# Performance work log

Hardware: AMD Instinct MI355X
Metric: run time of the kernel (lower is better)

The kernel has to match this reference:

```python
import jax, jax.numpy as jnp
import numpy as np

N_NODE = 40000
EMB = 100
LAYERS = 2
B = 512
L = 50
N = 50
E = 800000


def _l2norm(x, axis=-1, eps=1e-12):
    n = jnp.sqrt(jnp.sum(x * x, axis=axis, keepdims=True))
    return x / jnp.maximum(n, eps)


def _item_conv(rows, cols, vals, emb, b):
    # sparse A @ X repeated LAYERS times, stack, l2-normalize rows, weighted sum
    finals = [emb]
    x = emb
    for _ in range(LAYERS):
        x = jax.ops.segment_sum(vals[:, None] * x[cols], rows, num_segments=emb.shape[0])
        finals.append(x)
    f = _l2norm(jnp.stack(finals, 0))                      # [LAYERS+1, n, d]
    return jnp.sum(b[:, None, None] * f, axis=0)


def _session_conv(adj_dense, emb, a):
    finals = [emb]
    x = emb
    for _ in range(LAYERS):
        x = adj_dense @ x
        finals.append(x)
    f = _l2norm(jnp.stack(finals, 0))
    return jnp.sum(a[:, None, None] * f, axis=0)


def _gat(h, adj, a0, a1, a2, a3):
    # e_k[b,i,j] = leakyrelu(sum_d h[b,i,d]*h[b,j,d]*a_k[d]); never materialize [B,N,N,D]
    def score(a):
        return jax.nn.leaky_relu(jnp.einsum('bid,bjd->bij', h * a[:, 0], h), 0.2)
    e0, e1, e2, e3 = score(a0), score(a1), score(a2), score(a3)
    neg = jnp.float32(-9e15)
    alpha = jnp.where(adj == 1, e0, neg)
    alpha = jnp.where(adj == 2, e1, alpha)
    alpha = jnp.where(adj == 3, e2, alpha)
    alpha = jnp.where(adj == 4, e3, alpha)
    alpha = jax.nn.softmax(alpha, axis=-1)
    return jnp.einsum('bij,bjd->bid', alpha, h)


def _get_seq(emb_table, rev, h, alias, mix=0.8):
    seq_h = emb_table[rev]                                  # [B,L,D]
    bidx = jnp.arange(rev.shape[0])[:, None]
    seq_h_ = h[bidx, alias]                                 # [B,L,D]
    return (1.0 - mix) * seq_h + mix * seq_h_               # eval: dropout = identity


def _soft_attention(seq_h, mask_f, session_len, pos_emb, w1_W, w1_b, glu1_W, glu1_b, glu2_W, w2):
    hs = jnp.sum(seq_h, axis=1) / session_len               # [B,D]
    pos = jnp.broadcast_to(pos_emb[:seq_h.shape[1]][None], seq_h.shape)
    nh = jnp.tanh(jnp.concatenate([pos, seq_h], -1) @ w1_W.T + w1_b)
    nh = jax.nn.sigmoid(nh @ glu1_W.T + glu1_b + (hs @ glu2_W.T)[:, None, :])
    beta = (nh @ w2) * mask_f[..., None]                    # [B,L,1]
    return jnp.sum(beta * seq_h, axis=1)                    # [B,D]


def setup_inputs() -> dict:
    key = jax.random.key(0)
    ks = jax.random.split(key, 30)
    stdv = 1.0 / np.sqrt(EMB)
    u = lambda k, s: jax.random.uniform(k, s, jnp.float32, -stdv, stdv)
    return {
        'tar': jax.random.randint(ks[0], (B,), 0, N_NODE),
        'reversed_sess_item': jax.random.randint(ks[1], (B, L), 0, N_NODE + 1),
        'mask': jnp.ones((B, L), jnp.int32),
        'session_len': jnp.ones((B, 1), jnp.float32),
        'session_adj': jax.random.uniform(ks[2], (B, B), jnp.float32),
        'is_train': 0,
        'items': jax.random.randint(ks[3], (B, N), 0, N_NODE + 1),
        'adj': jax.random.randint(ks[4], (B, N, N), 0, 5),
        'alias_session': jax.random.randint(ks[5], (B, L), 0, N),
        'gnn_rows': jax.random.randint(ks[6], (E,), 0, N_NODE),
        'gnn_cols': jax.random.randint(ks[7], (E,), 0, N_NODE),
        'gnn_vals': jax.random.uniform(ks[8], (E,), jnp.float32),
        'nodes_emb': u(ks[9], (N_NODE, EMB)),
        'b_item': jnp.ones((LAYERS + 1,), jnp.float32),
        'a_sess': jnp.ones((LAYERS + 1,), jnp.float32),
        'a0': u(ks[10], (EMB, 1)), 'a1': u(ks[11], (EMB, 1)),
        'a2': u(ks[12], (EMB, 1)), 'a3': u(ks[13], (EMB, 1)),
        'w1_W': u(ks[14], (EMB, 2 * EMB)), 'w1_b': u(ks[15], (EMB,)),
        'w2': u(ks[16], (EMB, 1)),
        'glu1_W': u(ks[17], (EMB, EMB)), 'glu1_b': u(ks[18], (EMB,)),
        'glu2_W': u(ks[19], (EMB, EMB)),
        'pos_emb': u(ks[20], (150, EMB)),
    }


def reference(tar, reversed_sess_item, mask, session_len, session_adj, is_train,
              items, adj, alias_session, gnn_rows, gnn_cols, gnn_vals,
              nodes_emb, b_item, a_sess, a0, a1, a2, a3,
              w1_W, w1_b, w2, glu1_W, glu1_b, glu2_W, pos_emb):
    mask_f = mask.astype(jnp.float32)
    zeros = jnp.zeros((1, EMB), jnp.float32)
    emb_gnn = _item_conv(gnn_rows, gnn_cols, gnn_vals, nodes_emb, b_item)
    # eval mode: both dropouts are identity
    e1t = jnp.concatenate([zeros, emb_gnn], 0)
    e2t = jnp.concatenate([zeros, emb_gnn], 0)
    embeddings = e1t + e2t

    h1 = _gat(e1t[items], adj, a0, a1, a2, a3)
    h1 = _get_seq(e1t, reversed_sess_item, h1, alias_session, 0.8)
    h2 = _gat(e2t[items], adj, a0, a1, a2, a3)
    h2 = _get_seq(e2t, reversed_sess_item, h2, alias_session, 0.8)

    sel1 = _soft_attention(h1, mask_f, session_len, pos_emb, w1_W, w1_b, glu1_W, glu1_b, glu2_W, w2)
    sel1 = _session_conv(session_adj, sel1, a_sess)
    sel2 = _soft_attention(h2, mask_f, session_len, pos_emb, w1_W, w1_b, glu1_W, glu1_b, glu2_W, w2)
    sel2 = _session_conv(session_adj, sel2, a_sess)

    con_loss = jnp.float32(0.0)  # is_train == 0 (inference path)

    seq_h = sel1 + sel2
    scores = seq_h @ embeddings[1:].T                       # [B, N_NODE]
    logp = jax.nn.log_softmax(scores + 1e-8, axis=-1)
    loss = -jnp.mean(logp[jnp.arange(scores.shape[0]), tar])
    return (con_loss, loss, scores)
```

## Files before the change

### kernel.cpp

```cpp
#include <hip/hip_runtime.h>
#include <hip/hip_bf16.h>
#include <math.h>

#define N_NODE 40000
#define EMB 100
#define BB 512
#define LL 50
#define NI 50
#define EDG 800000
#define SCAN_BLOCKS 157

typedef short s16x8 __attribute__((ext_vector_type(8)));
typedef float f32x4 __attribute__((ext_vector_type(4)));

__global__ void khist(const int* __restrict__ rows, int* __restrict__ counts) {
  int e = blockIdx.x * 256 + threadIdx.x;
  atomicAdd(&counts[rows[e]], 1);
}

__global__ __launch_bounds__(256) void kscan1(const int* __restrict__ counts,
                                              int* __restrict__ scanout,
                                              int* __restrict__ blocksums, int n) {
  __shared__ int wsum[4];
  int tid = threadIdx.x;
  int i = blockIdx.x * 256 + tid;
  int v = (i < n) ? counts[i] : 0;
  int x = v;
  #pragma unroll
  for (int off = 1; off < 64; off <<= 1) {
    int t = __shfl_up(x, off, 64);
    if ((tid & 63) >= off) x += t;
  }
  int w = tid >> 6, lane = tid & 63;
  if (lane == 63) wsum[w] = x;
  __syncthreads();
  int woff = 0;
  #pragma unroll
  for (int k = 0; k < 4; ++k) woff += (k < w) ? wsum[k] : 0;
  int incl = x + woff;
  if (i < n) scanout[i] = incl - v;
  if (tid == 255) blocksums[blockIdx.x] = incl;
}

__global__ __launch_bounds__(256) void kscan2(int* __restrict__ blocksums, int nb) {
  __shared__ int wsum[4];
  int tid = threadIdx.x;
  int v = (tid < nb) ? blocksums[tid] : 0;
  int x = v;
  #pragma unroll
  for (int off = 1; off < 64; off <<= 1) {
    int t = __shfl_up(x, off, 64);
    if ((tid & 63) >= off) x += t;
  }
  int w = tid >> 6, lane = tid & 63;
  if (lane == 63) wsum[w] = x;
  __syncthreads();
  int woff = 0;
  #pragma unroll
  for (int k = 0; k < 4; ++k) woff += (k < w) ? wsum[k] : 0;
  if (tid < nb) blocksums[tid] = x + woff - v;
}

__global__ __launch_bounds__(256) void kscan3(const int* __restrict__ scanout,
                                              const int* __restrict__ blocksums,
                                              int* __restrict__ starts,
                                              int* __restrict__ cursor, int n) {
  int i = blockIdx.x * 256 + threadIdx.x;
  if (i < n) {
    int s = scanout[i] + blocksums[blockIdx.x];
    starts[i] = s;
    cursor[i] = s;
  }
}

__global__ void kfill(const int* __restrict__ rows, const int* __restrict__ cols,
                      const float* __restrict__ vals, int* __restrict__ cursor,
                      int* __restrict__ colS, float* __restrict__ valS) {
  int e = blockIdx.x * 256 + threadIdx.x;
  int r = rows[e];
  int p = atomicAdd(&cursor[r], 1);
  colS[p] = cols[e];
  valS[p] = vals[e];
}

__global__ __launch_bounds__(256) void kspmm(const int* __restrict__ starts,
                                             const int* __restrict__ counts,
                                             const int* __restrict__ colS,
                                             const float* __restrict__ valS,
                                             const float* __restrict__ x,
                                             float* __restrict__ out) {
  int row = blockIdx.x * 4 + (threadIdx.x >> 6);
  int lane = threadIdx.x & 63;
  int s = starts[row], cnt = counts[row];
  bool act = lane < 50;
  int d2 = (act ? lane : 49) * 2;
  float ax = 0.f, ay = 0.f;
  for (int base = 0; base < cnt; base += 64) {
    int nb = cnt - base; if (nb > 64) nb = 64;
    int cl = 0; float vl = 0.f;
    if (lane < nb) {
      cl = colS[s + base + lane];
      vl = valS[s + base + lane];
    }
    int t = 0;
    for (; t + 4 <= nb; t += 4) {
      int c0 = __shfl(cl, t),     c1 = __shfl(cl, t + 1);
      int c2 = __shfl(cl, t + 2), c3 = __shfl(cl, t + 3);
      float v0 = __shfl(vl, t),     v1 = __shfl(vl, t + 1);
      float v2 = __shfl(vl, t + 2), v3 = __shfl(vl, t + 3);
      float2 g0 = *(const float2*)(x + (size_t)c0 * EMB + d2);
      float2 g1 = *(const float2*)(x + (size_t)c1 * EMB + d2);
      float2 g2 = *(const float2*)(x + (size_t)c2 * EMB + d2);
      float2 g3 = *(const float2*)(x + (size_t)c3 * EMB + d2);
      ax += v0 * g0.x; ay += v0 * g0.y;
      ax += v1 * g1.x; ay += v1 * g1.y;
      ax += v2 * g2.x; ay += v2 * g2.y;
      ax += v3 * g3.x; ay += v3 * g3.y;
    }
    for (; t < nb; ++t) {
      int c = __shfl(cl, t);
      float v = __shfl(vl, t);
      float2 g = *(const float2*)(x + (size_t)c * EMB + d2);
      ax += v * g.x; ay += v * g.y;
    }
  }
  if (act) {
    float2 o; o.x = ax; o.y = ay;
    *(float2*)(out + (size_t)row * EMB + d2) = o;
  }
}

__global__ void kcomb(const float* __restrict__ x0, const float* __restrict__ x1,
                      const float* __restrict__ x2, const float* __restrict__ bI,
                      float* __restrict__ emb) {
  int n = blockIdx.x * 4 + (threadIdx.x >> 6);
  int lane = threadIdx.x & 63;
  int d0 = lane, d1 = lane + 64;
  bool h1 = d1 < EMB;
  size_t base = (size_t)n * EMB;
  float v00 = x0[base + d0], v01 = h1 ? x0[base + d1] : 0.f;
  float v10 = x1[base + d0], v11 = h1 ? x1[base + d1] : 0.f;
  float v20 = x2[base + d0], v21 = h1 ? x2[base + d1] : 0.f;
  float q0 = v00 * v00 + v01 * v01;
  float q1 = v10 * v10 + v11 * v11;
  float q2 = v20 * v20 + v21 * v21;
  #pragma unroll
  for (int off = 32; off; off >>= 1) {
    q0 += __shfl_xor(q0, off);
    q1 += __shfl_xor(q1, off);
    q2 += __shfl_xor(q2, off);
  }
  float r0 = 1.f / fmaxf(sqrtf(q0), 1e-12f);
  float r1 = 1.f / fmaxf(sqrtf(q1), 1e-12f);
  float r2 = 1.f / fmaxf(sqrtf(q2), 1e-12f);
  float b0 = bI[0], b1 = bI[1], b2 = bI[2];
  emb[base + d0] = b0 * v00 * r0 + b1 * v10 * r1 + b2 * v20 * r2;
  if (h1) emb[base + d1] = b0 * v01 * r0 + b1 * v11 * r1 + b2 * v21 * r2;
}

__global__ __launch_bounds__(256) void kgat(
    const float* __restrict__ emb, const int* __restrict__ items,
    const int* __restrict__ adj,
    const float* __restrict__ a0p, const float* __restrict__ a1p,
    const float* __restrict__ a2p, const float* __restrict__ a3p,
    float* __restrict__ hgat) {
  __shared__ __align__(16) float hl[64 * 108];
  __shared__ __align__(16) float as[4 * 100];
  __shared__ float al[4][4][64];
  int b = blockIdx.x;
  int tid = threadIdx.x;
  for (int idx = tid; idx < 400; idx += 256) {
    int k = idx / 100, d = idx % 100;
    const float* ap = (k == 0) ? a0p : (k == 1) ? a1p : (k == 2) ? a2p : a3p;
    as[idx] = ap[d];
  }
  for (int idx = tid; idx < 64 * 100; idx += 256) {
    int i = idx / 100, d = idx % 100;
    float v = 0.f;
    if (i < NI) {
      int node = items[b * NI + i];
      v = (node == 0) ? 0.f : emb[(size_t)(node - 1) * EMB + d];
    }
    hl[i * 108 + d] = v;
  }
  __syncthreads();
  int w = tid >> 6, lane = tid & 63;
  int i0 = w * 13;
  int nIw = 50 - i0; if (nIw > 13) nIw = 13;
  const float* hjrow = &hl[lane * 108];
  int u2 = lane >> 5, dq = lane & 31;
  int dqc = (dq < 25) ? dq : 24;
  for (int g = 0; g < nIw; g += 4) {
    int ib = i0 + g;
    int rem = nIw - g;
    int ir[4];
    #pragma unroll
    for (int u = 0; u < 4; ++u) { int i = ib + u; ir[u] = (i < NI) ? i : NI - 1; }
    float acck[4][4];
    #pragma unroll
    for (int u = 0; u < 4; ++u)
      #pragma unroll
      for (int k = 0; k < 4; ++k) acck[u][k] = 0.f;
    for (int d0 = 0; d0 < 100; d0 += 4) {
      float4 hj = *(const float4*)(hjrow + d0);
      float4 av0 = *(const float4*)&as[d0];
      float4 av1 = *(const float4*)&as[100 + d0];
      float4 av2 = *(const float4*)&as[200 + d0];
      float4 av3 = *(const float4*)&as[300 + d0];
      #pragma unroll
      for (int u = 0; u < 4; ++u) {
        float4 hi = *(const float4*)&hl[ir[u] * 108 + d0];
        float p0 = hi.x * hj.x, p1 = hi.y * hj.y;
        float p2 = hi.z * hj.z, p3 = hi.w * hj.w;
        acck[u][0] += p0 * av0.x + p1 * av0.y + p2 * av0.z + p3 * av0.w;
        acck[u][1] += p0 * av1.x + p1 * av1.y + p2 * av1.z + p3 * av1.w;
        acck[u][2] += p0 * av2.x + p1 * av2.y + p2 * av2.z + p3 * av2.w;
        acck[u][3] += p0 * av3.x + p1 * av3.y + p2 * av3.z + p3 * av3.w;
      }
    }
    #pragma unroll
    for (int u = 0; u < 4; ++u) {
      int i = ib + u;
      bool rowok = (u < rem);
      int av = 0;
      if (rowok && lane < NI) av = adj[(size_t)b * (NI * NI) + i * NI + lane];
      float sv = (av == 1) ? acck[u][0] : (av == 2) ? acck[u][1]
               : (av == 3) ? acck[u][2] : acck[u][3];
      sv = (sv >= 0.f) ? sv : 0.2f * sv;
      float e = (av == 0) ? -9e15f : sv;
      if (lane >= NI) e = -INFINITY;
      float m = e;
      #pragma unroll
      for (int off = 32; off; off >>= 1) m = fmaxf(m, __shfl_xor(m, off));
      float p = expf(e - m);
      float s = p;
      #pragma unroll
      for (int off = 32; off; off >>= 1) s += __shfl_xor(s, off);
      al[w][u][lane] = p / s;
    }
    #pragma unroll
    for (int pass = 0; pass < 2; ++pass) {
      int u = pass * 2 + u2;
      int i = ib + u;
      const float* alr = al[w][u];
      float ox = 0.f, oy = 0.f, oz = 0.f, ow = 0.f;
      for (int j = 0; j < NI; ++j) {
        float a = alr[j];
        float4 hv = *(const float4*)&hl[j * 108 + dqc * 4];
        ox += a * hv.x; oy += a * hv.y; oz += a * hv.z; ow += a * hv.w;
      }
      if (dq < 25 && u < rem) {
        float4 o4; o4.x = ox; o4.y = oy; o4.z = oz; o4.w = ow;
        *(float4*)&hgat[((size_t)b * NI + i) * EMB + dq * 4] = o4;
      }
    }
  }
}

__global__ void kseq(const float* __restrict__ emb, const int* __restrict__ rev,
                     const int* __restrict__ alias, const float* __restrict__ hgat,
                     float* __restrict__ hseq) {
  int idx = blockIdx.x * 256 + threadIdx.x;
  int b = idx / 5000, r = idx % 5000, l = r / 100, d = r % 100;
  int node = rev[b * LL + l];
  float sh = (node == 0) ? 0.f : emb[(size_t)(node - 1) * EMB + d];
  int a = alias[b * LL + l];
  float shh = hgat[((size_t)b * NI + a) * EMB + d];
  hseq[idx] = 0.2f * sh + 0.8f * shh;
}

__global__ void kprep_t(const float* __restrict__ w1W, const float* __restrict__ g1W,
                        const float* __restrict__ g2W, float* __restrict__ w1t2,
                        float* __restrict__ g1t, float* __restrict__ g2t) {
  int idx = blockIdx.x * 256 + threadIdx.x;
  if (idx >= 10000) return;
  int c = idx / 100, o = idx % 100;
  w1t2[c * 100 + o] = w1W[o * 200 + 100 + c];
  g1t[c * 100 + o] = g1W[o * 100 + c];
  g2t[c * 100 + o] = g2W[o * 100 + c];
}

__global__ void kprep_pos(const float* __restrict__ posE, const float* __restrict__ w1W,
                          const float* __restrict__ w1b, float* __restrict__ posW) {
  int idx = blockIdx.x * 256 + threadIdx.x;
  if (idx >= 5000) return;
  int l = idx / 100, o = idx % 100;
  float acc = w1b[o];
  for (int c = 0; c < 100; ++c) acc += posE[l * 100 + c] * w1W[o * 200 + c];
  posW[idx] = acc;
}

__global__ __launch_bounds__(256) void ksoft(
    const float* __restrict__ hseqG, const float* __restrict__ slenp,
    const int* __restrict__ maskp,
    const float* __restrict__ posW, const float* __restrict__ w1t2,
    const float* __restrict__ glu1t, const float* __restrict__ glu1b,
    const float* __restrict__ glu2t, const float* __restrict__ w2,
    float* __restrict__ sel) {
  __shared__ float hq[LL * 101];
  __shared__ float nh[LL * 100];
  __shared__ float red[25 * 52];
  __shared__ float hs_s[100];
  __shared__ float g_s[100];
  __shared__ float beta_s[LL];
  int b = blockIdx.x, tid = threadIdx.x;
  for (int idx = tid; idx < LL * 100; idx += 256) {
    int l = idx / 100, d = idx % 100;
    hq[l * 101 + d] = hseqG[((size_t)b * LL + l) * 100 + d];
  }
  __syncthreads();
  if (tid < 100) {
    float s = 0.f;
    for (int l = 0; l < LL; ++l) s += hq[l * 101 + tid];
    hs_s[tid] = s / slenp[b];
  }
  __syncthreads();
  if (tid < 100) {
    float acc = 0.f;
    for (int c = 0; c < 100; ++c) acc += hs_s[c] * glu2t[c * 100 + tid];
    g_s[tid] = acc;
  }
  int lg = tid / 25, og = tid % 25;
  if (tid < 250) {
    float acc[5][4];
    #pragma unroll
    for (int j = 0; j < 5; ++j) {
      float4 p = *(const float4*)&posW[(lg * 5 + j) * 100 + og * 4];
      acc[j][0] = p.x; acc[j][1] = p.y; acc[j][2] = p.z; acc[j][3] = p.w;
    }
    for (int c = 0; c < 100; ++c) {
      float4 wv = *(const float4*)&w1t2[c * 100 + og * 4];
      float hv[5];
      #pragma unroll
      for (int j = 0; j < 5; ++j) hv[j] = hq[(lg * 5 + j) * 101 + c];
      #pragma unroll
      for (int j = 0; j < 5; ++j) {
        acc[j][0] += hv[j] * wv.x;
        acc[j][1] += hv[j] * wv.y;
        acc[j][2] += hv[j] * wv.z;
        acc[j][3] += hv[j] * wv.w;
      }
    }
    #pragma unroll
    for (int j = 0; j < 5; ++j) {
      float4 t;
      t.x = tanhf(acc[j][0]); t.y = tanhf(acc[j][1]);
      t.z = tanhf(acc[j][2]); t.w = tanhf(acc[j][3]);
      *(float4*)&nh[(lg * 5 + j) * 100 + og * 4] = t;
    }
  }
  __syncthreads();
  if (tid < 250) {
    float4 gb = *(const float4*)&glu1b[og * 4];
    float4 gg = *(const float4*)&g_s[og * 4];
    float base0 = gg.x + gb.x, base1 = gg.y + gb.y, base2 = gg.z + gb.z, base3 = gg.w + gb.w;
    float acc[5][4];
    #pragma unroll
    for (int j = 0; j < 5; ++j) {
      acc[j][0] = base0; acc[j][1] = base1; acc[j][2] = base2; acc[j][3] = base3;
    }
    for (int c = 0; c < 100; ++c) {
      float4 wv = *(const float4*)&glu1t[c * 100 + og * 4];
      float hv[5];
      #pragma unroll
      for (int j = 0; j < 5; ++j) hv[j] = nh[(lg * 5 + j) * 100 + c];
      #pragma unroll
      for (int j = 0; j < 5; ++j) {
        acc[j][0] += hv[j] * wv.x;
        acc[j][1] += hv[j] * wv.y;
        acc[j][2] += hv[j] * wv.z;
        acc[j][3] += hv[j] * wv.w;
      }
    }
    float4 w2v = *(const float4*)&w2[og * 4];
    #pragma unroll
    for (int j = 0; j < 5; ++j) {
      float s0 = w2v.x / (1.f + expf(-acc[j][0]));
      float s1 = w2v.y / (1.f + expf(-acc[j][1]));
      float s2 = w2v.z / (1.f + expf(-acc[j][2]));
      float s3 = w2v.w / (1.f + expf(-acc[j][3]));
      red[og * 52 + lg * 5 + j] = (s0 + s1) + (s2 + s3);
    }
  }
  __syncthreads();
  if (tid < LL) {
    float s = 0.f;
    for (int og2 = 0; og2 < 25; ++og2) s += red[og2 * 52 + tid];
    beta_s[tid] = s * (float)maskp[b * LL + tid];
  }
  __syncthreads();
  if (tid < 100) {
    float acc = 0.f;
    for (int l = 0; l < LL; ++l) acc += beta_s[l] * hq[l * 101 + tid];
    sel[(size_t)b * 100 + tid] = acc;
  }
}

__global__ void ksess(const float* __restrict__ adjS, const float* __restrict__ x,
                      float* __restrict__ out) {
  int b = blockIdx.x, d = threadIdx.x;
  if (d >= 100) return;
  const float* ar = adjS + (size_t)b * BB;
  float a0 = 0.f, a1 = 0.f, a2 = 0.f, a3 = 0.f;
  for (int j = 0; j < BB; j += 4) {
    a0 += ar[j]     * x[(j)     * 100 + d];
    a1 += ar[j + 1] * x[(j + 1) * 100 + d];
    a2 += ar[j + 2] * x[(j + 2) * 100 + d];
    a3 += ar[j + 3] * x[(j + 3) * 100 + d];
  }
  out[(size_t)b * 100 + d] = (a0 + a1) + (a2 + a3);
}

__global__ void ksesscomb(const float* __restrict__ x0, const float* __restrict__ x1,
                          const float* __restrict__ x2, const float* __restrict__ aS,
                          float* __restrict__ out) {
  int b = blockIdx.x * 4 + (threadIdx.x >> 6);
  int lane = threadIdx.x & 63;
  int d0 = lane, d1 = lane + 64;
  bool h1 = d1 < EMB;
  size_t base = (size_t)b * EMB;
  float v00 = x0[base + d0], v01 = h1 ? x0[base + d1] : 0.f;
  float v10 = x1[base + d0], v11 = h1 ? x1[base + d1] : 0.f;
  float v20 = x2[base + d0], v21 = h1 ? x2[base + d1] : 0.f;
  float q0 = v00 * v00 + v01 * v01;
  float q1 = v10 * v10 + v11 * v11;
  float q2 = v20 * v20 + v21 * v21;
  #pragma unroll
  for (int off = 32; off; off >>= 1) {
    q0 += __shfl_xor(q0, off);
    q1 += __shfl_xor(q1, off);
    q2 += __shfl_xor(q2, off);
  }
  float r0 = 1.f / fmaxf(sqrtf(q0), 1e-12f);
  float r1 = 1.f / fmaxf(sqrtf(q1), 1e-12f);
  float r2 = 1.f / fmaxf(sqrtf(q2), 1e-12f);
  float b0 = aS[0], b1 = aS[1], b2 = aS[2];
  out[base + d0] = 2.f * (b0 * v00 * r0 + b1 * v10 * r1 + b2 * v20 * r2);
  if (h1) out[base + d1] = 2.f * (b0 * v01 * r0 + b1 * v11 * r1 + b2 * v21 * r2);
}

__global__ void kprepB(const float* __restrict__ emb, unsigned short* __restrict__ bHi,
                       unsigned short* __restrict__ bLo) {
  int idx = blockIdx.x * 256 + threadIdx.x;
  int n = idx >> 7, k = idx & 127;
  float v = (k < EMB) ? 2.f * emb[(size_t)n * EMB + k] : 0.f;
  __hip_bfloat16 h = __float2bfloat16(v);
  float rem = v - __bfloat162float(h);
  __hip_bfloat16 l = __float2bfloat16(rem);
  bHi[idx] = *reinterpret_cast<unsigned short*>(&h);
  bLo[idx] = *reinterpret_cast<unsigned short*>(&l);
}

__global__ void kprepA(const float* __restrict__ seqh, unsigned short* __restrict__ aHi,
                       unsigned short* __restrict__ aLo) {
  int idx = blockIdx.x * 256 + threadIdx.x;
  int n = idx >> 7, k = idx & 127;
  float v = (k < EMB) ? seqh[(size_t)n * EMB + k] : 0.f;
  __hip_bfloat16 h = __float2bfloat16(v);
  float rem = v - __bfloat162float(h);
  __hip_bfloat16 l = __float2bfloat16(rem);
  aHi[idx] = *reinterpret_cast<unsigned short*>(&h);
  aLo[idx] = *reinterpret_cast<unsigned short*>(&l);
}

__global__ __launch_bounds__(256) void kscoresM(
    const unsigned short* __restrict__ aHi, const unsigned short* __restrict__ aLo,
    const unsigned short* __restrict__ bHi, const unsigned short* __restrict__ bLo,
    float* __restrict__ outS) {
  __shared__ __align__(16) unsigned short Bh[64 * 136];
  __shared__ __align__(16) unsigned short Bl[64 * 136];
  int tid = threadIdx.x;
  int n0 = blockIdx.x * 64, b0 = blockIdx.y * 64;
  int w = tid >> 6, lane = tid & 63;
  int ln = lane & 15, quad = lane >> 4;

  const unsigned short* aRowH = aHi + (size_t)(b0 + w * 16 + ln) * 128 + quad * 8;
  const unsigned short* aRowL = aLo + (size_t)(b0 + w * 16 + ln) * 128 + quad * 8;
  s16x8 ah[4], al[4];
  #pragma unroll
  for (int s = 0; s < 4; ++s) {
    ah[s] = *(const s16x8*)(aRowH + s * 32);
    al[s] = *(const s16x8*)(aRowL + s * 32);
  }

  #pragma unroll
  for (int it = 0; it < 4; ++it) {
    int seg = tid + it * 256;
    int r = seg >> 4, q = seg & 15;
    *(s16x8*)&Bh[r * 136 + q * 8] = *(const s16x8*)&bHi[(size_t)(n0 + r) * 128 + q * 8];
    *(s16x8*)&Bl[r * 136 + q * 8] = *(const s16x8*)&bLo[(size_t)(n0 + r) * 128 + q * 8];
  }
  __syncthreads();

  f32x4 acc[4];
  #pragma unroll
  for (int t = 0; t < 4; ++t) acc[t] = (f32x4){0.f, 0.f, 0.f, 0.f};

  #pragma unroll
  for (int s = 0; s < 4; ++s) {
    #pragma unroll
    for (int t = 0; t < 4; ++t) {
      s16x8 bh = *(const s16x8*)&Bh[(t * 16 + ln) * 136 + s * 32 + quad * 8];
      s16x8 bl = *(const s16x8*)&Bl[(t * 16 + ln) * 136 + s * 32 + quad * 8];
      acc[t] = __builtin_amdgcn_mfma_f32_16x16x32_bf16(ah[s], bh, acc[t], 0, 0, 0);
      acc[t] = __builtin_amdgcn_mfma_f32_16x16x32_bf16(al[s], bh, acc[t], 0, 0, 0);
      acc[t] = __builtin_amdgcn_mfma_f32_16x16x32_bf16(ah[s], bl, acc[t], 0, 0, 0);
    }
  }

  int brow = b0 + w * 16 + quad * 4;
  #pragma unroll
  for (int t = 0; t < 4; ++t) {
    int ncol = n0 + t * 16 + ln;
    #pragma unroll
    for (int r = 0; r < 4; ++r) {
      outS[(size_t)(brow + r) * N_NODE + ncol] = acc[t][r];
    }
  }
}

__global__ __launch_bounds__(256) void klse(const float* __restrict__ outS,
                                            const int* __restrict__ tar,
                                            float* __restrict__ part) {
  __shared__ float ms[256], ss[256];
  int b = blockIdx.x, tid = threadIdx.x;
  const float2* sp = (const float2*)(outS + (size_t)b * N_NODE);
  float m = -INFINITY, s = 0.f;
  for (int i = tid; i < N_NODE / 2; i += 256) {
    float2 v = sp[i];
    float mx = fmaxf(v.x, v.y);
    float add = expf(v.x - mx) + expf(v.y - mx);
    if (mx > m) { s = s * expf(m - mx) + add; m = mx; }
    else s += add * expf(mx - m);
  }
  ms[tid] = m; ss[tid] = s;
  __syncthreads();
  for (int st = 128; st; st >>= 1) {
    if (tid < st) {
      float m2 = ms[tid + st], s2 = ss[tid + st];
      float M = fmaxf(ms[tid], m2);
      ss[tid] = ss[tid] * expf(ms[tid] - M) + s2 * expf(m2 - M);
      ms[tid] = M;
    }
    __syncthreads();
  }
  if (tid == 0) {
    float tsc = outS[(size_t)b * N_NODE + tar[b]];
    part[b] = tsc - (ms[0] + logf(ss[0]));
  }
}

__global__ void kfinal(const float* __restrict__ part, float* __restrict__ out) {
  __shared__ float red[256];
  int tid = threadIdx.x;
  red[tid] = part[tid] + part[tid + 256];
  __syncthreads();
  for (int st = 128; st; st >>= 1) {
    if (tid < st) red[tid] += red[tid + st];
    __syncthreads();
  }
  if (tid == 0) {
    out[0] = 0.f;
    out[1] = -red[0] / (float)BB;
  }
}

extern "C" void kernel_launch(void* const* d_in, const int* in_sizes, int n_in,
                              void* d_out, int out_size, void* d_ws, size_t ws_size,
                              hipStream_t stream) {
  const int* tar    = (const int*)d_in[0];
  const int* rev    = (const int*)d_in[1];
  const int* maskp  = (const int*)d_in[2];
  const float* slen = (const float*)d_in[3];
  const float* sadj = (const float*)d_in[4];
  const int* items  = (const int*)d_in[6];
  const int* adjp   = (const int*)d_in[7];
  const int* alias  = (const int*)d_in[8];
  const int* grows  = (const int*)d_in[9];
  const int* gcols  = (const int*)d_in[10];
  const float* gvals = (const float*)d_in[11];
  const float* nemb = (const float*)d_in[12];
  const float* bI   = (const float*)d_in[13];
  const float* aS   = (const float*)d_in[14];
  const float* a0p  = (const float*)d_in[15];
  const float* a1p  = (const float*)d_in[16];
  const float* a2p  = (const float*)d_in[17];
  const float* a3p  = (const float*)d_in[18];
  const float* w1W  = (const float*)d_in[19];
  const float* w1b  = (const float*)d_in[20];
  const float* w2p  = (const float*)d_in[21];
  const float* g1W  = (const float*)d_in[22];
  const float* g1b  = (const float*)d_in[23];
  const float* g2W  = (const float*)d_in[24];
  const float* posE = (const float*)d_in[25];

  float* W = (float*)d_ws;
  size_t o = 0;
  float* emb_gnn = W + o; o += (size_t)N_NODE * EMB;
  float* x1      = W + o; o += (size_t)N_NODE * EMB;
  float* x2      = W + o; o += (size_t)N_NODE * EMB;
  float* sel     = W + o; o += (size_t)BB * EMB;
  float* y1      = W + o; o += (size_t)BB * EMB;
  float* y2      = W + o; o += (size_t)BB * EMB;
  float* seqh    = W + o; o += (size_t)BB * EMB;
  float* posW    = W + o; o += 5120;
  float* w1t2    = W + o; o += 10000;
  float* glu1t   = W + o; o += 10000;
  float* glu2t   = W + o; o += 10000;
  float* valS    = W + o; o += EDG;
  float* part    = W + o; o += 512;
  int* colS   = (int*)(W + o); o += EDG;
  int* counts = (int*)(W + o); o += N_NODE;
  int* starts = (int*)(W + o); o += N_NODE;
  int* cursor = (int*)(W + o); o += N_NODE;
  int* scantmp = (int*)(W + o); o += N_NODE;
  int* blocksums = (int*)(W + o); o += 256;
  unsigned short* aHi = (unsigned short*)(W + o); o += 32768;
  unsigned short* aLo = (unsigned short*)(W + o); o += 32768;
  float* hgat = x1;
  float* hseq = x2;
  unsigned short* bHi = (unsigned short*)x1;
  unsigned short* bLo = (unsigned short*)x2;

  float* outF = (float*)d_out;
  float* outScores = outF + 2;

  hipMemsetAsync(counts, 0, N_NODE * sizeof(int), stream);
  khist<<<EDG / 256, 256, 0, stream>>>(grows, counts);
  kscan1<<<SCAN_BLOCKS, 256, 0, stream>>>(counts, scantmp, blocksums, N_NODE);
  kscan2<<<1, 256, 0, stream>>>(blocksums, SCAN_BLOCKS);
  kscan3<<<SCAN_BLOCKS, 256, 0, stream>>>(scantmp, blocksums, starts, cursor, N_NODE);
  kfill<<<EDG / 256, 256, 0, stream>>>(grows, gcols, gvals, cursor, colS, valS);
  kspmm<<<N_NODE / 4, 256, 0, stream>>>(starts, counts, colS, valS, nemb, x1);
  kspmm<<<N_NODE / 4, 256, 0, stream>>>(starts, counts, colS, valS, x1, x2);
  kcomb<<<N_NODE / 4, 256, 0, stream>>>(nemb, x1, x2, bI, emb_gnn);
  kgat<<<BB, 256, 0, stream>>>(emb_gnn, items, adjp, a0p, a1p, a2p, a3p, hgat);
  kseq<<<(BB * LL * EMB) / 256, 256, 0, stream>>>(emb_gnn, rev, alias, hgat, hseq);
  kprep_t<<<40, 256, 0, stream>>>(w1W, g1W, g2W, w1t2, glu1t, glu2t);
  kprep_pos<<<20, 256, 0, stream>>>(posE, w1W, w1b, posW);
  ksoft<<<BB, 256, 0, stream>>>(hseq, slen, maskp, posW, w1t2, glu1t, g1b, glu2t, w2p, sel);
  kprepB<<<(N_NODE * 128) / 256, 256, 0, stream>>>(emb_gnn, bHi, bLo);
  ksess<<<BB, 128, 0, stream>>>(sadj, sel, y1);
  ksess<<<BB, 128, 0, stream>>>(sadj, y1, y2);
  ksesscomb<<<BB / 4, 256, 0, stream>>>(sel, y1, y2, aS, seqh);
  kprepA<<<(BB * 128) / 256, 256, 0, stream>>>(seqh, aHi, aLo);
  kscoresM<<<dim3(N_NODE / 64, BB / 64), 256, 0, stream>>>(aHi, aLo, bHi, bLo, outScores);
  klse<<<BB, 256, 0, stream>>>(outScores, tar, part);
  kfinal<<<1, 256, 0, stream>>>(part, outF);
}
```

Baseline: 582.4 us.

## Split GAT rows across two blocks and compute only the selected attention score

The GAT kernel now launches two blocks per session, each handling 25 query rows, which doubles the number of blocks available to fill the GPU. It reads the adjacency type before the dot product and accumulates only the one score that type selects, instead of all four weighted variants. Embedding rows are loaded as float2. In exchange, each block reloads the full session embedding tile, and the selected weight vector is read per lane through a pointer that can diverge across lanes.

```diff
diff --git a/kernel.cpp b/kernel.cpp
--- a/kernel.cpp
+++ b/kernel.cpp
@@ -167,67 +167,60 @@
   __shared__ __align__(16) float hl[64 * 108];
   __shared__ __align__(16) float as[4 * 100];
   __shared__ float al[4][4][64];
-  int b = blockIdx.x;
+  int b = blockIdx.x, half = blockIdx.y;
   int tid = threadIdx.x;
   for (int idx = tid; idx < 400; idx += 256) {
     int k = idx / 100, d = idx % 100;
     const float* ap = (k == 0) ? a0p : (k == 1) ? a1p : (k == 2) ? a2p : a3p;
     as[idx] = ap[d];
   }
-  for (int idx = tid; idx < 64 * 100; idx += 256) {
-    int i = idx / 100, d = idx % 100;
-    float v = 0.f;
+  for (int idx = tid; idx < 64 * 50; idx += 256) {
+    int i = idx / 50, d2 = (idx % 50) * 2;
+    float2 v; v.x = 0.f; v.y = 0.f;
     if (i < NI) {
       int node = items[b * NI + i];
-      v = (node == 0) ? 0.f : emb[(size_t)(node - 1) * EMB + d];
-    }
-    hl[i * 108 + d] = v;
+      if (node != 0) v = *(const float2*)(emb + (size_t)(node - 1) * EMB + d2);
+    }
+    *(float2*)&hl[i * 108 + d2] = v;
   }
   __syncthreads();
   int w = tid >> 6, lane = tid & 63;
-  int i0 = w * 13;
-  int nIw = 50 - i0; if (nIw > 13) nIw = 13;
+  int i0 = half * 25 + w * 7;
+  int nIw = 25 - w * 7; if (nIw > 7) nIw = 7;
   const float* hjrow = &hl[lane * 108];
   int u2 = lane >> 5, dq = lane & 31;
   int dqc = (dq < 25) ? dq : 24;
   for (int g = 0; g < nIw; g += 4) {
     int ib = i0 + g;
     int rem = nIw - g;
-    int ir[4];
-    #pragma unroll
-    for (int u = 0; u < 4; ++u) { int i = ib + u; ir[u] = (i < NI) ? i : NI - 1; }
-    float acck[4][4];
-    #pragma unroll
-    for (int u = 0; u < 4; ++u)
-      #pragma unroll
-      for (int k = 0; k < 4; ++k) acck[u][k] = 0.f;
+    int ir[4], av[4];
+    const float* asel[4];
+    #pragma unroll
+    for (int u = 0; u < 4; ++u) {
+      int i = ib + u; ir[u] = (i < NI) ? i : NI - 1;
+      av[u] = (lane < NI) ? adj[(size_t)b * (NI * NI) + ir[u] * NI + lane] : 0;
+      int k = av[u] - 1; if (k < 0) k = 0; if (k > 3) k = 3;
+      asel[u] = &as[k * 100];
+    }
+    float acc[4];
+    #pragma unroll
+    for (int u = 0; u < 4; ++u) acc[u] = 0.f;
     for (int d0 = 0; d0 < 100; d0 += 4) {
       float4 hj = *(const float4*)(hjrow + d0);
-      float4 av0 = *(const float4*)&as[d0];
-      float4 av1 = *(const float4*)&as[100 + d0];
-      float4 av2 = *(const float4*)&as[200 + d0];
-      float4 av3 = *(const float4*)&as[300 + d0];
       #pragma unroll
       for (int u = 0; u < 4; ++u) {
         float4 hi = *(const float4*)&hl[ir[u] * 108 + d0];
+        float4 aw = *(const float4*)(asel[u] + d0);
         float p0 = hi.x * hj.x, p1 = hi.y * hj.y;
         float p2 = hi.z * hj.z, p3 = hi.w * hj.w;
-        acck[u][0] += p0 * av0.x + p1 * av0.y + p2 * av0.z + p3 * av0.w;
-        acck[u][1] += p0 * av1.x + p1 * av1.y + p2 * av1.z + p3 * av1.w;
-        acck[u][2] += p0 * av2.x + p1 * av2.y + p2 * av2.z + p3 * av2.w;
-        acck[u][3] += p0 * av3.x + p1 * av3.y + p2 * av3.z + p3 * av3.w;
+        acc[u] += p0 * aw.x + p1 * aw.y + p2 * aw.z + p3 * aw.w;
       }
     }
     #pragma unroll
     for (int u = 0; u < 4; ++u) {
-      int i = ib + u;
-      bool rowok = (u < rem);
-      int av = 0;
-      if (rowok && lane < NI) av = adj[(size_t)b * (NI * NI) + i * NI + lane];
-      float sv = (av == 1) ? acck[u][0] : (av == 2) ? acck[u][1]
-               : (av == 3) ? acck[u][2] : acck[u][3];
+      float sv = acc[u];
       sv = (sv >= 0.f) ? sv : 0.2f * sv;
-      float e = (av == 0) ? -9e15f : sv;
+      float e = (av[u] == 0) ? -9e15f : sv;
       if (lane >= NI) e = -INFINITY;
       float m = e;
       #pragma unroll
@@ -634,7 +627,7 @@
   kspmm<<<N_NODE / 4, 256, 0, stream>>>(starts, counts, colS, valS, nemb, x1);
   kspmm<<<N_NODE / 4, 256, 0, stream>>>(starts, counts, colS, valS, x1, x2);
   kcomb<<<N_NODE / 4, 256, 0, stream>>>(nemb, x1, x2, bI, emb_gnn);
-  kgat<<<BB, 256, 0, stream>>>(emb_gnn, items, adjp, a0p, a1p, a2p, a3p, hgat);
+  kgat<<<dim3(BB, 2), 256, 0, stream>>>(emb_gnn, items, adjp, a0p, a1p, a2p, a3p, hgat);
   kseq<<<(BB * LL * EMB) / 256, 256, 0, stream>>>(emb_gnn, rev, alias, hgat, hseq);
   kprep_t<<<40, 256, 0, stream>>>(w1W, g1W, g2W, w1t2, glu1t, glu2t);
   kprep_pos<<<20, 256, 0, stream>>>(posE, w1W, w1b, posW);
```

Result: faster. 566.3 us (-2.8%).
